# Kernel optimization log

Hardware: AMD Instinct MI355X
Metric: run time of the kernel (lower is better)

Reference implementation:

```python
import jax, jax.numpy as jnp
import numpy as np

N, E = 50000, 600000
DIN, D, C = 239, 128, 2
NEG_SLOPE_MLP = 0.01   # nn.LeakyReLU default
NEG_SLOPE_ATT = 0.2    # GATConv default


def leaky(x, s):
    return jnp.where(x >= 0, x, s * x)


def setup_inputs() -> dict:
    key = jax.random.key(0)
    ks = jax.random.split(key, 12)
    sc = lambda d: 1.0 / np.sqrt(d)
    return {
        "x": jax.random.normal(ks[0], (N, DIN), jnp.float32),
        "edge_index": jax.random.randint(ks[1], (2, E), 0, N, jnp.int32),
        "edge_type": jax.random.randint(ks[2], (E,), 0, 4, jnp.int32),
        "W_in": jax.random.normal(ks[3], (DIN, D), jnp.float32) * sc(DIN),
        "b_in": jnp.zeros((D,), jnp.float32),
        "W_gat": jax.random.normal(ks[4], (D, D), jnp.float32) * sc(D),
        "att_src": jax.random.normal(ks[5], (D,), jnp.float32) * sc(D),
        "att_dst": jax.random.normal(ks[6], (D,), jnp.float32) * sc(D),
        "b_gat": jnp.zeros((D,), jnp.float32),
        "W_h": jax.random.normal(ks[7], (D, D), jnp.float32) * sc(D),
        "b_h": jnp.zeros((D,), jnp.float32),
        "W_out": jax.random.normal(ks[8], (D, C), jnp.float32) * sc(D),
        "b_out": jnp.zeros((C,), jnp.float32),
    }


def reference(x, edge_index, edge_type, W_in, b_in, W_gat, att_src, att_dst,
              b_gat, W_h, b_h, W_out, b_out):
    # input encoder: Linear + LeakyReLU
    h = leaky(x @ W_in + b_in, NEG_SLOPE_MLP)                      # [N, D]

    # GATConv (heads=1): add self loops, edge attention, segment softmax over dst
    loops = jnp.arange(N, dtype=edge_index.dtype)
    src = jnp.concatenate([edge_index[0], loops])                  # [E+N]
    dst = jnp.concatenate([edge_index[1], loops])

    g = h @ W_gat                                                  # [N, D]
    a_src = g @ att_src                                            # [N]
    a_dst = g @ att_dst                                            # [N]
    e = leaky(a_src[src] + a_dst[dst], NEG_SLOPE_ATT)              # [E+N]

    m = jax.ops.segment_max(e, dst, num_segments=N)                # self-loops => no empty segs
    w = jnp.exp(e - m[dst])
    z = jax.ops.segment_sum(w, dst, num_segments=N)
    alpha = w / z[dst]                                             # [E+N]

    out = jax.ops.segment_sum(alpha[:, None] * g[src], dst, num_segments=N) + b_gat

    # dropout is identity in eval mode
    h2 = leaky(out @ W_h + b_h, NEG_SLOPE_MLP)
    return h2 @ W_out + b_out                                      # [N, C]
```

## Files before the change

### kernel.cpp

```cpp
#include <hip/hip_runtime.h>

#define NNODE 50000
#define NEDGE 600000
#define KDIN  239
#define DDIM  128
#define NTILES 3125
#define NBG   782
#define NBUCK 256
#define BSZ   196
#define NPB   128
#define CHP   4688

typedef _Float16 half8 __attribute__((ext_vector_type(8)));
typedef _Float16 half4 __attribute__((ext_vector_type(4)));
typedef __attribute__((ext_vector_type(4))) float f32x4;

__device__ __forceinline__ ushort f2h(float f){
  union { _Float16 h; ushort u; } c; c.h = (_Float16)f; return c.u;
}

__global__ __launch_bounds__(256) void pre_k(
    const float* __restrict__ W_in, const float* __restrict__ W_gat, const float* __restrict__ W_h,
    ushort* __restrict__ BfA, ushort* __restrict__ BfB, ushort* __restrict__ BfC,
    const int* __restrict__ ei, int* __restrict__ cpart)
{
  __shared__ int hb[NBUCK];
  const int b = blockIdx.x, t = threadIdx.x;
  if (b < NPB){
    hb[t] = 0;
    __syncthreads();
    const int e0 = b*CHP, e1 = min(NEDGE, e0+CHP);
    for (int e=e0+t; e<e1; e+=256){
      int dst = min(max(ei[NEDGE+e],0), NNODE-1);
      atomicAdd(&hb[dst/BSZ], 1);
    }
    __syncthreads();
    cpart[b*NBUCK + t] = hb[t];
  } else if (b < NPB + 128){
    int idx = (b-NPB)*256 + t; int n = idx >> 8, k = idx & 255;
    BfA[idx] = (k < KDIN) ? f2h(W_in[(size_t)k*DDIM + n]) : (ushort)0;
  } else if (b < NPB + 192){
    int idx = (b-NPB-128)*256 + t; int n = idx >> 7, k = idx & 127;
    BfB[idx] = f2h(W_gat[(size_t)k*DDIM + n]);
  } else {
    int idx = (b-NPB-192)*256 + t; int n = idx >> 7, k = idx & 127;
    BfC[idx] = f2h(W_h[(size_t)k*DDIM + n]);
  }
}

__global__ __launch_bounds__(256) void scan_k(int* __restrict__ cpart)
{
  __shared__ int sc[NBUCK];
  const int t = threadIdx.x;
  int tot = 0;
  #pragma unroll 8
  for (int i=0;i<NPB;i++) tot += cpart[i*NBUCK + t];
  sc[t] = tot;
  __syncthreads();
  #pragma unroll
  for (int off=1; off<NBUCK; off<<=1){
    int v = (t>=off) ? sc[t-off] : 0;
    __syncthreads();
    sc[t] += v;
    __syncthreads();
  }
  int run = sc[t] - tot;
  #pragma unroll 8
  for (int i=0;i<NPB;i++){
    int c = cpart[i*NBUCK + t];
    cpart[i*NBUCK + t] = run;
    run += c;
  }
}

__global__ __launch_bounds__(256, 3) void gemmAB_k(
    const float* __restrict__ x, const ushort* __restrict__ BfA,
    const ushort* __restrict__ BfB, const float* __restrict__ b_in,
    ushort* __restrict__ gf,
    const float* __restrict__ vs, const float* __restrict__ vd,
    float* __restrict__ os, float* __restrict__ od,
    float* __restrict__ bms, float* __restrict__ bmd,
    const int* __restrict__ ei, const int* __restrict__ cpart, int* __restrict__ pairs)
{
  __shared__ __attribute__((aligned(16))) ushort Bs[128*128];
  __shared__ __attribute__((aligned(16))) ushort ht[4][16*128];
  if (blockIdx.x < NPB){
    int* cur = (int*)Bs;
    const int pb = blockIdx.x;
    cur[threadIdx.x] = cpart[pb*NBUCK + threadIdx.x];
    __syncthreads();
    const int e0 = pb*CHP, e1 = min(NEDGE, e0+CHP);
    for (int e=e0+threadIdx.x; e<e1; e+=256){
      int dst = min(max(ei[NEDGE+e],0), NNODE-1);
      int src = min(max(ei[e],0), NNODE-1);
      int bk = (unsigned)dst / BSZ;
      int pos = atomicAdd(&cur[bk], 1);
      pairs[pos] = src | ((dst - bk*BSZ) << 16);
    }
    return;
  }
  const int lane = threadIdx.x & 63;
  const int wave = threadIdx.x >> 6;
  const int q = lane >> 4, c = lane & 15;
  const int tile = (blockIdx.x - NPB)*4 + wave;
  const bool act = tile < NTILES;
  const int rowBase = tile*16;
  const int swz = (c&7)<<4;
  f32x4 acc[8];
  half8 af[8];
  if (act){
    const float* __restrict__ ap = x + (size_t)(rowBase + c)*KDIN;
    #pragma unroll
    for (int s=0;s<7;s++){
      const float* __restrict__ p = ap + s*32 + q*8;
      #pragma unroll
      for (int i=0;i<8;i++) af[s][i] = (_Float16)p[i];
    }
    #pragma unroll
    for (int i=0;i<8;i++){
      const int k = 224 + q*8 + i;
      af[7][i] = (_Float16)((k < KDIN) ? ap[k] : 0.f);
    }
    #pragma unroll
    for (int t=0;t<8;t++) acc[t] = (f32x4){0.f,0.f,0.f,0.f};
  }
  #pragma unroll
  for (int H=0; H<2; ++H){
    #pragma unroll
    for (int it=0; it<8; ++it){
      const int idx = it*256 + threadIdx.x;
      const int row = idx >> 4, sl = (idx & 15)*16;
      const half8 v = *(const half8*)(BfA + (size_t)row*256 + H*128 + (idx & 15)*8);
      *(half8*)((char*)Bs + row*256 + (sl ^ ((row&7)<<4))) = v;
    }
    __syncthreads();
    if (act){
      const char* __restrict__ bsl = (const char*)Bs + c*256;
      #pragma unroll
      for (int s=0;s<4;s++){
        const int so = (s*64 + q*16) ^ swz;
        #pragma unroll
        for (int t=0;t<8;t++){
          const half8 bf = *(const half8*)(bsl + t*16*256 + so);
          acc[t] = __builtin_amdgcn_mfma_f32_16x16x32_f16(af[H*4+s], bf, acc[t], 0,0,0);
        }
      }
    }
    __syncthreads();
  }
  if (act){
    char* __restrict__ hw = (char*)&ht[wave][0];
    #pragma unroll
    for (int t=0;t<8;t++){
      const int col = 16*t + c;
      const float bv = b_in[col];
      #pragma unroll
      for (int r=0;r<4;r++){
        const int row = q*4 + r;
        float v = acc[t][r] + bv;
        v = (v >= 0.f) ? v : 0.01f*v;
        *(_Float16*)(hw + ((row*256 + col*2) ^ ((row&7)<<4))) = (_Float16)v;
      }
    }
  }
  #pragma unroll
  for (int it=0; it<8; ++it){
    const int idx = it*256 + threadIdx.x;
    const int row = idx >> 4, sl = (idx & 15)*16;
    const half8 v = *(const half8*)(BfB + (size_t)idx*8);
    *(half8*)((char*)Bs + row*256 + (sl ^ ((row&7)<<4))) = v;
  }
  __syncthreads();
  if (!act) return;
  half8 af2[4];
  const char* __restrict__ hr = (const char*)&ht[wave][0] + c*256;
  #pragma unroll
  for (int s=0;s<4;s++) af2[s] = *(const half8*)(hr + ((s*64 + q*16) ^ swz));
  #pragma unroll
  for (int t=0;t<8;t++) acc[t] = (f32x4){0.f,0.f,0.f,0.f};
  const char* __restrict__ bsl2 = (const char*)Bs + c*256;
  #pragma unroll
  for (int s=0;s<4;s++){
    const int so = (s*64 + q*16) ^ swz;
    #pragma unroll
    for (int t=0;t<8;t++){
      const half8 bf = *(const half8*)(bsl2 + t*16*256 + so);
      acc[t] = __builtin_amdgcn_mfma_f32_16x16x32_f16(af2[s], bf, acc[t], 0,0,0);
    }
  }
  float pr0[4] = {0,0,0,0}, pr1[4] = {0,0,0,0};
  #pragma unroll
  for (int t=0;t<8;t++){
    const int col = 16*t + c;
    const float va = vs[col], vb = vd[col];
    #pragma unroll
    for (int r=0;r<4;r++){
      const int row = rowBase + q*4 + r;
      const float v = acc[t][r];
      gf[(size_t)row*DDIM + col] = f2h(v);
      pr0[r] += v*va; pr1[r] += v*vb;
    }
  }
  float lmax_s = -3.0e38f, lmax_d = -3.0e38f;
  #pragma unroll
  for (int r=0;r<4;r++){
    float s0 = pr0[r], s1 = pr1[r];
    s0 += __shfl_xor(s0,8); s1 += __shfl_xor(s1,8);
    s0 += __shfl_xor(s0,4); s1 += __shfl_xor(s1,4);
    s0 += __shfl_xor(s0,2); s1 += __shfl_xor(s1,2);
    s0 += __shfl_xor(s0,1); s1 += __shfl_xor(s1,1);
    lmax_s = fmaxf(lmax_s, s0); lmax_d = fmaxf(lmax_d, s1);
    if (c == 0){
      const int row = rowBase + q*4 + r;
      os[row] = s0; od[row] = s1;
    }
  }
  #pragma unroll
  for (int off=32; off>0; off>>=1){
    lmax_s = fmaxf(lmax_s, __shfl_xor(lmax_s, off));
    lmax_d = fmaxf(lmax_d, __shfl_xor(lmax_d, off));
  }
  if (lane == 0){ bms[tile] = lmax_s; bmd[tile] = lmax_d; }
}

__global__ __launch_bounds__(256, 4) void gemmC_k(
    const ushort* __restrict__ Af, const ushort* __restrict__ Btf,
    const float* __restrict__ bias, float* __restrict__ outf,
    const float* __restrict__ Wo, const float* __restrict__ bo)
{
  constexpr int Kpad = 128, Kb = 256;
  __shared__ __attribute__((aligned(16))) ushort Bs[128*Kpad];
  #pragma unroll
  for (int it=0; it<8; ++it){
    const int idx = it*256 + threadIdx.x;
    const int row = idx >> 4, sl = (idx & 15)*16;
    const half8 v = *(const half8*)(Btf + (size_t)idx*8);
    *(half8*)((char*)Bs + row*Kb + (sl ^ ((row&7)<<4))) = v;
  }
  __syncthreads();
  const int lane = threadIdx.x & 63;
  const int wave = threadIdx.x >> 6;
  const int q = lane >> 4, c = lane & 15;
  const int tile = blockIdx.x*4 + wave;
  if (tile >= NTILES) return;
  const int rowBase = tile*16;
  half8 af[4];
  const ushort* __restrict__ ap = Af + (size_t)(rowBase + c)*Kpad + q*8;
  #pragma unroll
  for (int s=0;s<4;s++) af[s] = *(const half8*)(ap + s*32);
  f32x4 acc[8];
  #pragma unroll
  for (int t=0;t<8;t++) acc[t] = (f32x4){0.f,0.f,0.f,0.f};
  const int swz = (c&7)<<4;
  const char* __restrict__ bsl = (const char*)Bs + c*Kb;
  #pragma unroll
  for (int s=0;s<4;s++){
    const int so = (s*64 + q*16) ^ swz;
    #pragma unroll
    for (int t=0;t<8;t++){
      const half8 bf = *(const half8*)(bsl + t*16*Kb + so);
      acc[t] = __builtin_amdgcn_mfma_f32_16x16x32_f16(af[s], bf, acc[t], 0,0,0);
    }
  }
  float pr0[4] = {0,0,0,0}, pr1[4] = {0,0,0,0};
  #pragma unroll
  for (int t=0;t<8;t++){
    const int col = 16*t + c;
    const float bv = bias[col];
    const float va = Wo[2*col], vb = Wo[2*col+1];
    #pragma unroll
    for (int r=0;r<4;r++){
      float v = acc[t][r] + bv;
      v = (v >= 0.f) ? v : 0.01f*v;
      pr0[r] += v*va; pr1[r] += v*vb;
    }
  }
  #pragma unroll
  for (int r=0;r<4;r++){
    float s0 = pr0[r], s1 = pr1[r];
    s0 += __shfl_xor(s0,8); s1 += __shfl_xor(s1,8);
    s0 += __shfl_xor(s0,4); s1 += __shfl_xor(s1,4);
    s0 += __shfl_xor(s0,2); s1 += __shfl_xor(s1,2);
    s0 += __shfl_xor(s0,1); s1 += __shfl_xor(s1,1);
    if (c == 0){
      const int row = rowBase + q*4 + r;
      float2 y2; y2.x = s0 + bo[0]; y2.y = s1 + bo[1];
      *(float2*)&outf[(size_t)row*2] = y2;
    }
  }
}

__global__ __launch_bounds__(256) void fine_k(const int* __restrict__ pairs,
    const int* __restrict__ cpart, int* __restrict__ offs, int* __restrict__ degv,
    int* __restrict__ es, const float* __restrict__ bms, const float* __restrict__ bmd,
    float* __restrict__ gmf)
{
  __shared__ int fh[256];
  __shared__ int sc[256];
  const int b = blockIdx.x, t = threadIdx.x;
  if (b == NBUCK){
    float ms = -3.0e38f, md = -3.0e38f;
    for (int i=t; i<NTILES; i+=256){ ms = fmaxf(ms, bms[i]); md = fmaxf(md, bmd[i]); }
    #pragma unroll
    for (int off=32; off>0; off>>=1){
      ms = fmaxf(ms, __shfl_xor(ms, off));
      md = fmaxf(md, __shfl_xor(md, off));
    }
    float* red = (float*)fh;
    const int w = t >> 6;
    if ((t & 63) == 0){ red[w] = ms; red[4+w] = md; }
    __syncthreads();
    if (t == 0){
      gmf[0] = fmaxf(fmaxf(red[0],red[1]), fmaxf(red[2],red[3]));
      gmf[1] = fmaxf(fmaxf(red[4],red[5]), fmaxf(red[6],red[7]));
    }
    return;
  }
  const int s0 = cpart[b];
  const int s1 = (b < NBUCK-1) ? cpart[b+1] : NEDGE;
  fh[t] = 0;
  __syncthreads();
  for (int i=s0+t; i<s1; i+=256)
    atomicAdd(&fh[pairs[i] >> 16], 1);
  __syncthreads();
  const int deg = fh[t];
  sc[t] = deg;
  __syncthreads();
  #pragma unroll
  for (int off=1; off<256; off<<=1){
    int v = (t>=off) ? sc[t-off] : 0;
    __syncthreads();
    sc[t] += v;
    __syncthreads();
  }
  const int excl = sc[t] - deg;
  const int dst = b*BSZ + t;
  if (t < BSZ && dst < NNODE){ offs[dst] = s0 + excl; degv[dst] = deg; }
  fh[t] = s0 + excl;
  __syncthreads();
  for (int i=s0+t; i<s1; i+=256){
    const int p = pairs[i];
    const int pos = atomicAdd(&fh[p >> 16], 1);
    es[pos] = p & 0xFFFF;
  }
}

__global__ __launch_bounds__(256) void agg_k(const ushort* __restrict__ gf,
    const int* __restrict__ offs, const int* __restrict__ degv,
    const int* __restrict__ es,
    const float* __restrict__ a_src, const float* __restrict__ a_dst,
    const float* __restrict__ gmf, const float* __restrict__ b_gat,
    ushort* __restrict__ og)
{
  const int lane = threadIdx.x & 63;
  const int half = lane >> 5, li = lane & 31;
  const int dst = blockIdx.x*8 + (threadIdx.x >> 6)*2 + half;
  if (dst >= NNODE) return;
  float M = gmf[0] + gmf[1];
  M = (M >= 0.f) ? M : 0.2f*M;
  const int start = offs[dst];
  const int deg = degv[dst];
  const int* __restrict__ bin = es + start;
  const float ad = a_dst[dst];
  f32x4 a0={0,0,0,0}, a1={0,0,0,0}, a2={0,0,0,0}, a3={0,0,0,0};
  float w0s=0.f, w1s=0.f, w2s=0.f, w3s=0.f;
  int j = 0;
  for (; j+3 < deg; j += 4){
    const int i0=bin[j], i1=bin[j+1], i2=bin[j+2], i3=bin[j+3];
    float e0=a_src[i0]+ad; e0=(e0>=0.f)?e0:0.2f*e0;
    float e1=a_src[i1]+ad; e1=(e1>=0.f)?e1:0.2f*e1;
    float e2=a_src[i2]+ad; e2=(e2>=0.f)?e2:0.2f*e2;
    float e3=a_src[i3]+ad; e3=(e3>=0.f)?e3:0.2f*e3;
    const float w0=__expf(e0-M), w1=__expf(e1-M), w2=__expf(e2-M), w3=__expf(e3-M);
    const half4 g0 = *(const half4*)(gf + (size_t)i0*DDIM + li*4);
    const half4 g1 = *(const half4*)(gf + (size_t)i1*DDIM + li*4);
    const half4 g2 = *(const half4*)(gf + (size_t)i2*DDIM + li*4);
    const half4 g3 = *(const half4*)(gf + (size_t)i3*DDIM + li*4);
    #pragma unroll
    for (int i=0;i<4;i++){
      a0[i] += w0*(float)g0[i]; a1[i] += w1*(float)g1[i];
      a2[i] += w2*(float)g2[i]; a3[i] += w3*(float)g3[i];
    }
    w0s += w0; w1s += w1; w2s += w2; w3s += w3;
  }
  for (; j < deg; ++j){
    const int si = bin[j];
    float e0=a_src[si]+ad; e0=(e0>=0.f)?e0:0.2f*e0;
    const float w = __expf(e0-M);
    const half4 gv = *(const half4*)(gf + (size_t)si*DDIM + li*4);
    #pragma unroll
    for (int i=0;i<4;i++) a0[i] += w*(float)gv[i];
    w0s += w;
  }
  {
    float evs=a_src[dst]+ad; evs=(evs>=0.f)?evs:0.2f*evs;
    const float w = __expf(evs-M);
    const half4 gv = *(const half4*)(gf + (size_t)dst*DDIM + li*4);
    #pragma unroll
    for (int i=0;i<4;i++) a0[i] += w*(float)gv[i];
    w0s += w;
  }
  const float inv = 1.f/(w0s+w1s+w2s+w3s);
  const float4 bg = *(const float4*)&b_gat[li*4];
  ushort4 o;
  o.x = f2h((a0[0]+a1[0]+a2[0]+a3[0])*inv + bg.x);
  o.y = f2h((a0[1]+a1[1]+a2[1]+a3[1])*inv + bg.y);
  o.z = f2h((a0[2]+a1[2]+a2[2]+a3[2])*inv + bg.z);
  o.w = f2h((a0[3]+a1[3]+a2[3]+a3[3])*inv + bg.w);
  *(ushort4*)(og + (size_t)dst*DDIM + li*4) = o;
}

extern "C" void kernel_launch(void* const* d_in, const int* in_sizes, int n_in,
                              void* d_out, int out_size, void* d_ws, size_t ws_size,
                              hipStream_t stream)
{
  const float* x       = (const float*)d_in[0];
  const int*   ei      = (const int*)d_in[1];
  const float* W_in    = (const float*)d_in[3];
  const float* b_in    = (const float*)d_in[4];
  const float* W_gat   = (const float*)d_in[5];
  const float* att_src = (const float*)d_in[6];
  const float* att_dst = (const float*)d_in[7];
  const float* b_gat   = (const float*)d_in[8];
  const float* W_h     = (const float*)d_in[9];
  const float* b_h     = (const float*)d_in[10];
  const float* W_out   = (const float*)d_in[11];
  const float* b_out   = (const float*)d_in[12];

  char* ws = (char*)d_ws;
  ushort*   gf     = (ushort*)  (ws + 12800000);
  ushort*   og     = (ushort*)  (ws + 25600000);
  ushort*   BfA    = (ushort*)  (ws + 38400000);
  ushort*   BfB    = (ushort*)  (ws + 38600000);
  ushort*   BfC    = (ushort*)  (ws + 38700000);
  int*      cpart  = (int*)     (ws + 38800000);
  int*      pairs  = (int*)     (ws + 39100000);
  int*      es     = (int*)     (ws + 41500000);
  int*      offs   = (int*)     (ws + 43900000);
  int*      degv   = (int*)     (ws + 44100000);
  float*    a_src  = (float*)   (ws + 44300000);
  float*    a_dst  = (float*)   (ws + 44500000);
  float*    gm     = (float*)   (ws + 44700000);
  float*    bmaxS  = (float*)   (ws + 44700032);
  float*    bmaxD  = (float*)   (ws + 44712544);

  pre_k<<<NPB + 256, 256, 0, stream>>>(W_in, W_gat, W_h, BfA, BfB, BfC, ei, cpart);
  scan_k<<<1, 256, 0, stream>>>(cpart);
  gemmAB_k<<<NPB + NBG, 256, 0, stream>>>(x, BfA, BfB, b_in, gf,
      att_src, att_dst, a_src, a_dst, bmaxS, bmaxD, ei, cpart, pairs);
  fine_k<<<NBUCK + 1, 256, 0, stream>>>(pairs, cpart, offs, degv, es, bmaxS, bmaxD, gm);
  agg_k<<<6250, 256, 0, stream>>>(gf, offs, degv, es, a_src, a_dst, gm, b_gat, og);
  gemmC_k<<<NBG, 256, 0, stream>>>(og, BfC, b_h, (float*)d_out, W_out, b_out);
}
```

Before: 180.9 us.

## Fuse GAT aggregation with final MLP GEMM through shared-memory tile

Merges the edge aggregation kernel and the final hidden GEMM kernel into one kernel. Each wave aggregates 16 destination rows into a swizzled LDS tile, then runs MFMA against W_h and the output projection directly. This removes the fp16 round trip of the aggregated features through global memory and one kernel launch. In exchange, the aggregation now runs over 782 blocks with 8 sequential row iterations per wave and more LDS per block, which reduces parallelism and latency hiding for the irregular gathers.

```diff
diff --git a/kernel.cpp b/kernel.cpp
--- a/kernel.cpp
+++ b/kernel.cpp
@@ -223,42 +223,159 @@
   if (lane == 0){ bms[tile] = lmax_s; bmd[tile] = lmax_d; }
 }
 
-__global__ __launch_bounds__(256, 4) void gemmC_k(
-    const ushort* __restrict__ Af, const ushort* __restrict__ Btf,
-    const float* __restrict__ bias, float* __restrict__ outf,
-    const float* __restrict__ Wo, const float* __restrict__ bo)
-{
-  constexpr int Kpad = 128, Kb = 256;
-  __shared__ __attribute__((aligned(16))) ushort Bs[128*Kpad];
+__global__ __launch_bounds__(256) void fine_k(const int* __restrict__ pairs,
+    const int* __restrict__ cpart, int* __restrict__ offs, int* __restrict__ degv,
+    int* __restrict__ es, const float* __restrict__ bms, const float* __restrict__ bmd,
+    float* __restrict__ gmf)
+{
+  __shared__ int fh[256];
+  __shared__ int sc[256];
+  const int b = blockIdx.x, t = threadIdx.x;
+  if (b == NBUCK){
+    float ms = -3.0e38f, md = -3.0e38f;
+    for (int i=t; i<NTILES; i+=256){ ms = fmaxf(ms, bms[i]); md = fmaxf(md, bmd[i]); }
+    #pragma unroll
+    for (int off=32; off>0; off>>=1){
+      ms = fmaxf(ms, __shfl_xor(ms, off));
+      md = fmaxf(md, __shfl_xor(md, off));
+    }
+    float* red = (float*)fh;
+    const int w = t >> 6;
+    if ((t & 63) == 0){ red[w] = ms; red[4+w] = md; }
+    __syncthreads();
+    if (t == 0){
+      gmf[0] = fmaxf(fmaxf(red[0],red[1]), fmaxf(red[2],red[3]));
+      gmf[1] = fmaxf(fmaxf(red[4],red[5]), fmaxf(red[6],red[7]));
+    }
+    return;
+  }
+  const int s0 = cpart[b];
+  const int s1 = (b < NBUCK-1) ? cpart[b+1] : NEDGE;
+  fh[t] = 0;
+  __syncthreads();
+  for (int i=s0+t; i<s1; i+=256)
+    atomicAdd(&fh[pairs[i] >> 16], 1);
+  __syncthreads();
+  const int deg = fh[t];
+  sc[t] = deg;
+  __syncthreads();
+  #pragma unroll
+  for (int off=1; off<256; off<<=1){
+    int v = (t>=off) ? sc[t-off] : 0;
+    __syncthreads();
+    sc[t] += v;
+    __syncthreads();
+  }
+  const int excl = sc[t] - deg;
+  const int dst = b*BSZ + t;
+  if (t < BSZ && dst < NNODE){ offs[dst] = s0 + excl; degv[dst] = deg; }
+  fh[t] = s0 + excl;
+  __syncthreads();
+  for (int i=s0+t; i<s1; i+=256){
+    const int p = pairs[i];
+    const int pos = atomicAdd(&fh[p >> 16], 1);
+    es[pos] = p & 0xFFFF;
+  }
+}
+
+__global__ __launch_bounds__(256, 3) void aggC_k(const ushort* __restrict__ gf,
+    const int* __restrict__ offs, const int* __restrict__ degv,
+    const int* __restrict__ es,
+    const float* __restrict__ a_src, const float* __restrict__ a_dst,
+    const float* __restrict__ gmf, const float* __restrict__ b_gat,
+    const ushort* __restrict__ BfC, const float* __restrict__ b_h,
+    const float* __restrict__ Wo, const float* __restrict__ bo,
+    float* __restrict__ outf)
+{
+  __shared__ __attribute__((aligned(16))) ushort Bs[128*128];
+  __shared__ __attribute__((aligned(16))) ushort ot[4][16*128];
   #pragma unroll
   for (int it=0; it<8; ++it){
     const int idx = it*256 + threadIdx.x;
     const int row = idx >> 4, sl = (idx & 15)*16;
-    const half8 v = *(const half8*)(Btf + (size_t)idx*8);
-    *(half8*)((char*)Bs + row*Kb + (sl ^ ((row&7)<<4))) = v;
+    const half8 v = *(const half8*)(BfC + (size_t)idx*8);
+    *(half8*)((char*)Bs + row*256 + (sl ^ ((row&7)<<4))) = v;
   }
   __syncthreads();
   const int lane = threadIdx.x & 63;
   const int wave = threadIdx.x >> 6;
-  const int q = lane >> 4, c = lane & 15;
+  const int slot = lane >> 5, li = lane & 31;
   const int tile = blockIdx.x*4 + wave;
   if (tile >= NTILES) return;
   const int rowBase = tile*16;
+  float M = gmf[0] + gmf[1];
+  M = (M >= 0.f) ? M : 0.2f*M;
+  char* __restrict__ ow = (char*)&ot[wave][0];
+  const float4 bg = *(const float4*)&b_gat[li*4];
+  for (int it=0; it<8; ++it){
+    const int d = it*2 + slot;
+    const int dst = rowBase + d;
+    const int start = offs[dst];
+    const int dg = degv[dst];
+    const int* __restrict__ bin = es + start;
+    const float ad = a_dst[dst];
+    f32x4 a0={0,0,0,0}, a1={0,0,0,0}, a2={0,0,0,0}, a3={0,0,0,0};
+    float w0s=0.f, w1s=0.f, w2s=0.f, w3s=0.f;
+    int j = 0;
+    for (; j+3 < dg; j += 4){
+      const int i0=bin[j], i1=bin[j+1], i2=bin[j+2], i3=bin[j+3];
+      float e0=a_src[i0]+ad; e0=(e0>=0.f)?e0:0.2f*e0;
+      float e1=a_src[i1]+ad; e1=(e1>=0.f)?e1:0.2f*e1;
+      float e2=a_src[i2]+ad; e2=(e2>=0.f)?e2:0.2f*e2;
+      float e3=a_src[i3]+ad; e3=(e3>=0.f)?e3:0.2f*e3;
+      const float w0=__expf(e0-M), w1=__expf(e1-M), w2=__expf(e2-M), w3=__expf(e3-M);
+      const half4 g0 = *(const half4*)(gf + (size_t)i0*DDIM + li*4);
+      const half4 g1 = *(const half4*)(gf + (size_t)i1*DDIM + li*4);
+      const half4 g2 = *(const half4*)(gf + (size_t)i2*DDIM + li*4);
+      const half4 g3 = *(const half4*)(gf + (size_t)i3*DDIM + li*4);
+      #pragma unroll
+      for (int i=0;i<4;i++){
+        a0[i] += w0*(float)g0[i]; a1[i] += w1*(float)g1[i];
+        a2[i] += w2*(float)g2[i]; a3[i] += w3*(float)g3[i];
+      }
+      w0s += w0; w1s += w1; w2s += w2; w3s += w3;
+    }
+    for (; j < dg; ++j){
+      const int si = bin[j];
+      float e0=a_src[si]+ad; e0=(e0>=0.f)?e0:0.2f*e0;
+      const float w = __expf(e0-M);
+      const half4 gv = *(const half4*)(gf + (size_t)si*DDIM + li*4);
+      #pragma unroll
+      for (int i=0;i<4;i++) a0[i] += w*(float)gv[i];
+      w0s += w;
+    }
+    {
+      float evs=a_src[dst]+ad; evs=(evs>=0.f)?evs:0.2f*evs;
+      const float w = __expf(evs-M);
+      const half4 gv = *(const half4*)(gf + (size_t)dst*DDIM + li*4);
+      #pragma unroll
+      for (int i=0;i<4;i++) a0[i] += w*(float)gv[i];
+      w0s += w;
+    }
+    const float inv = 1.f/(w0s+w1s+w2s+w3s);
+    half4 o;
+    o[0] = (_Float16)((a0[0]+a1[0]+a2[0]+a3[0])*inv + bg.x);
+    o[1] = (_Float16)((a0[1]+a1[1]+a2[1]+a3[1])*inv + bg.y);
+    o[2] = (_Float16)((a0[2]+a1[2]+a2[2]+a3[2])*inv + bg.z);
+    o[3] = (_Float16)((a0[3]+a1[3]+a2[3]+a3[3])*inv + bg.w);
+    *(half4*)(ow + ((d*256 + li*8) ^ ((d&7)<<4))) = o;
+  }
+  const int q = lane >> 4, c = lane & 15;
+  const int swz = (c&7)<<4;
   half8 af[4];
-  const ushort* __restrict__ ap = Af + (size_t)(rowBase + c)*Kpad + q*8;
-  #pragma unroll
-  for (int s=0;s<4;s++) af[s] = *(const half8*)(ap + s*32);
+  const char* __restrict__ hr = ow + c*256;
+  #pragma unroll
+  for (int s=0;s<4;s++) af[s] = *(const half8*)(hr + ((s*64 + q*16) ^ swz));
   f32x4 acc[8];
   #pragma unroll
   for (int t=0;t<8;t++) acc[t] = (f32x4){0.f,0.f,0.f,0.f};
-  const int swz = (c&7)<<4;
-  const char* __restrict__ bsl = (const char*)Bs + c*Kb;
+  const char* __restrict__ bsl = (const char*)Bs + c*256;
   #pragma unroll
   for (int s=0;s<4;s++){
     const int so = (s*64 + q*16) ^ swz;
     #pragma unroll
     for (int t=0;t<8;t++){
-      const half8 bf = *(const half8*)(bsl + t*16*Kb + so);
+      const half8 bf = *(const half8*)(bsl + t*16*256 + so);
       acc[t] = __builtin_amdgcn_mfma_f32_16x16x32_f16(af[s], bf, acc[t], 0,0,0);
     }
   }
@@ -266,7 +383,7 @@
   #pragma unroll
   for (int t=0;t<8;t++){
     const int col = 16*t + c;
-    const float bv = bias[col];
+    const float bv = b_h[col];
     const float va = Wo[2*col], vb = Wo[2*col+1];
     #pragma unroll
     for (int r=0;r<4;r++){
@@ -288,126 +405,6 @@
       *(float2*)&outf[(size_t)row*2] = y2;
     }
   }
-}
-
-__global__ __launch_bounds__(256) void fine_k(const int* __restrict__ pairs,
-    const int* __restrict__ cpart, int* __restrict__ offs, int* __restrict__ degv,
-    int* __restrict__ es, const float* __restrict__ bms, const float* __restrict__ bmd,
-    float* __restrict__ gmf)
-{
-  __shared__ int fh[256];
-  __shared__ int sc[256];
-  const int b = blockIdx.x, t = threadIdx.x;
-  if (b == NBUCK){
-    float ms = -3.0e38f, md = -3.0e38f;
-    for (int i=t; i<NTILES; i+=256){ ms = fmaxf(ms, bms[i]); md = fmaxf(md, bmd[i]); }
-    #pragma unroll
-    for (int off=32; off>0; off>>=1){
-      ms = fmaxf(ms, __shfl_xor(ms, off));
-      md = fmaxf(md, __shfl_xor(md, off));
-    }
-    float* red = (float*)fh;
-    const int w = t >> 6;
-    if ((t & 63) == 0){ red[w] = ms; red[4+w] = md; }
-    __syncthreads();
-    if (t == 0){
-      gmf[0] = fmaxf(fmaxf(red[0],red[1]), fmaxf(red[2],red[3]));
-      gmf[1] = fmaxf(fmaxf(red[4],red[5]), fmaxf(red[6],red[7]));
-    }
-    return;
-  }
-  const int s0 = cpart[b];
-  const int s1 = (b < NBUCK-1) ? cpart[b+1] : NEDGE;
-  fh[t] = 0;
-  __syncthreads();
-  for (int i=s0+t; i<s1; i+=256)
-    atomicAdd(&fh[pairs[i] >> 16], 1);
-  __syncthreads();
-  const int deg = fh[t];
-  sc[t] = deg;
-  __syncthreads();
-  #pragma unroll
-  for (int off=1; off<256; off<<=1){
-    int v = (t>=off) ? sc[t-off] : 0;
-    __syncthreads();
-    sc[t] += v;
-    __syncthreads();
-  }
-  const int excl = sc[t] - deg;
-  const int dst = b*BSZ + t;
-  if (t < BSZ && dst < NNODE){ offs[dst] = s0 + excl; degv[dst] = deg; }
-  fh[t] = s0 + excl;
-  __syncthreads();
-  for (int i=s0+t; i<s1; i+=256){
-    const int p = pairs[i];
-    const int pos = atomicAdd(&fh[p >> 16], 1);
-    es[pos] = p & 0xFFFF;
-  }
-}
-
-__global__ __launch_bounds__(256) void agg_k(const ushort* __restrict__ gf,
-    const int* __restrict__ offs, const int* __restrict__ degv,
-    const int* __restrict__ es,
-    const float* __restrict__ a_src, const float* __restrict__ a_dst,
-    const float* __restrict__ gmf, const float* __restrict__ b_gat,
-    ushort* __restrict__ og)
-{
-  const int lane = threadIdx.x & 63;
-  const int half = lane >> 5, li = lane & 31;
-  const int dst = blockIdx.x*8 + (threadIdx.x >> 6)*2 + half;
-  if (dst >= NNODE) return;
-  float M = gmf[0] + gmf[1];
-  M = (M >= 0.f) ? M : 0.2f*M;
-  const int start = offs[dst];
-  const int deg = degv[dst];
-  const int* __restrict__ bin = es + start;
-  const float ad = a_dst[dst];
-  f32x4 a0={0,0,0,0}, a1={0,0,0,0}, a2={0,0,0,0}, a3={0,0,0,0};
-  float w0s=0.f, w1s=0.f, w2s=0.f, w3s=0.f;
-  int j = 0;
-  for (; j+3 < deg; j += 4){
-    const int i0=bin[j], i1=bin[j+1], i2=bin[j+2], i3=bin[j+3];
-    float e0=a_src[i0]+ad; e0=(e0>=0.f)?e0:0.2f*e0;
-    float e1=a_src[i1]+ad; e1=(e1>=0.f)?e1:0.2f*e1;
-    float e2=a_src[i2]+ad; e2=(e2>=0.f)?e2:0.2f*e2;
-    float e3=a_src[i3]+ad; e3=(e3>=0.f)?e3:0.2f*e3;
-    const float w0=__expf(e0-M), w1=__expf(e1-M), w2=__expf(e2-M), w3=__expf(e3-M);
-    const half4 g0 = *(const half4*)(gf + (size_t)i0*DDIM + li*4);
-    const half4 g1 = *(const half4*)(gf + (size_t)i1*DDIM + li*4);
-    const half4 g2 = *(const half4*)(gf + (size_t)i2*DDIM + li*4);
-    const half4 g3 = *(const half4*)(gf + (size_t)i3*DDIM + li*4);
-    #pragma unroll
-    for (int i=0;i<4;i++){
-      a0[i] += w0*(float)g0[i]; a1[i] += w1*(float)g1[i];
-      a2[i] += w2*(float)g2[i]; a3[i] += w3*(float)g3[i];
-    }
-    w0s += w0; w1s += w1; w2s += w2; w3s += w3;
-  }
-  for (; j < deg; ++j){
-    const int si = bin[j];
-    float e0=a_src[si]+ad; e0=(e0>=0.f)?e0:0.2f*e0;
-    const float w = __expf(e0-M);
-    const half4 gv = *(const half4*)(gf + (size_t)si*DDIM + li*4);
-    #pragma unroll
-    for (int i=0;i<4;i++) a0[i] += w*(float)gv[i];
-    w0s += w;
-  }
-  {
-    float evs=a_src[dst]+ad; evs=(evs>=0.f)?evs:0.2f*evs;
-    const float w = __expf(evs-M);
-    const half4 gv = *(const half4*)(gf + (size_t)dst*DDIM + li*4);
-    #pragma unroll
-    for (int i=0;i<4;i++) a0[i] += w*(float)gv[i];
-    w0s += w;
-  }
-  const float inv = 1.f/(w0s+w1s+w2s+w3s);
-  const float4 bg = *(const float4*)&b_gat[li*4];
-  ushort4 o;
-  o.x = f2h((a0[0]+a1[0]+a2[0]+a3[0])*inv + bg.x);
-  o.y = f2h((a0[1]+a1[1]+a2[1]+a3[1])*inv + bg.y);
-  o.z = f2h((a0[2]+a1[2]+a2[2]+a3[2])*inv + bg.z);
-  o.w = f2h((a0[3]+a1[3]+a2[3]+a3[3])*inv + bg.w);
-  *(ushort4*)(og + (size_t)dst*DDIM + li*4) = o;
 }
 
 extern "C" void kernel_launch(void* const* d_in, const int* in_sizes, int n_in,
@@ -428,27 +425,26 @@
   const float* b_out   = (const float*)d_in[12];
 
   char* ws = (char*)d_ws;
-  ushort*   gf     = (ushort*)  (ws + 12800000);
-  ushort*   og     = (ushort*)  (ws + 25600000);
-  ushort*   BfA    = (ushort*)  (ws + 38400000);
-  ushort*   BfB    = (ushort*)  (ws + 38600000);
-  ushort*   BfC    = (ushort*)  (ws + 38700000);
-  int*      cpart  = (int*)     (ws + 38800000);
-  int*      pairs  = (int*)     (ws + 39100000);
-  int*      es     = (int*)     (ws + 41500000);
-  int*      offs   = (int*)     (ws + 43900000);
-  int*      degv   = (int*)     (ws + 44100000);
-  float*    a_src  = (float*)   (ws + 44300000);
-  float*    a_dst  = (float*)   (ws + 44500000);
-  float*    gm     = (float*)   (ws + 44700000);
-  float*    bmaxS  = (float*)   (ws + 44700032);
-  float*    bmaxD  = (float*)   (ws + 44712544);
+  ushort*   gf     = (ushort*)  (ws + 0);
+  ushort*   BfA    = (ushort*)  (ws + 12800000);
+  ushort*   BfB    = (ushort*)  (ws + 13000000);
+  ushort*   BfC    = (ushort*)  (ws + 13100000);
+  int*      cpart  = (int*)     (ws + 13200000);
+  int*      pairs  = (int*)     (ws + 13500000);
+  int*      es     = (int*)     (ws + 15900000);
+  int*      offs   = (int*)     (ws + 18300000);
+  int*      degv   = (int*)     (ws + 18500000);
+  float*    a_src  = (float*)   (ws + 18700000);
+  float*    a_dst  = (float*)   (ws + 18900000);
+  float*    gm     = (float*)   (ws + 19100000);
+  float*    bmaxS  = (float*)   (ws + 19100064);
+  float*    bmaxD  = (float*)   (ws + 19116064);
 
   pre_k<<<NPB + 256, 256, 0, stream>>>(W_in, W_gat, W_h, BfA, BfB, BfC, ei, cpart);
   scan_k<<<1, 256, 0, stream>>>(cpart);
   gemmAB_k<<<NPB + NBG, 256, 0, stream>>>(x, BfA, BfB, b_in, gf,
       att_src, att_dst, a_src, a_dst, bmaxS, bmaxD, ei, cpart, pairs);
   fine_k<<<NBUCK + 1, 256, 0, stream>>>(pairs, cpart, offs, degv, es, bmaxS, bmaxD, gm);
-  agg_k<<<6250, 256, 0, stream>>>(gf, offs, degv, es, a_src, a_dst, gm, b_gat, og);
-  gemmC_k<<<NBG, 256, 0, stream>>>(og, BfC, b_h, (float*)d_out, W_out, b_out);
-}
+  aggC_k<<<NBG, 256, 0, stream>>>(gf, offs, degv, es, a_src, a_dst, gm, b_gat,
+      BfC, b_h, W_out, b_out, (float*)d_out);
+}
```

After: 220.8 us. 1.22x slower.
